# Kernel tuning notes

Measured on AMD Instinct MI355X. Metric: run time of the kernel, lower is better.

Reference implementation:

```python
import jax, jax.numpy as jnp
import numpy as np

POOL = 3      # pooling_size
EPS = 0.006   # constant added to each segment mean in the original code


def setup_inputs() -> dict:
    key = jax.random.key(0)
    k1, k2 = jax.random.split(key)
    B, N, D = 8, 3072, 1024          # N divisible by POOL -> no remainder branch
    steps = N // POOL
    x = jax.random.normal(k1, (B, N, D), dtype=jnp.float32)
    # (start, end) shot boundaries, sorted so start <= end, values in [0, N)
    graph = jnp.sort(jax.random.randint(k2, (B, steps, 2), 0, N, dtype=jnp.int64), axis=-1)
    return {"x": x, "graph": graph}


def reference(x, graph):
    B, N, D = x.shape
    steps = N // POOL
    # Exclusive+inclusive prefix sums: c[b, k] = sum over x[b, :k]  -> [B, N+1, D]
    c = jnp.concatenate([jnp.zeros((B, 1, D), x.dtype), jnp.cumsum(x, axis=1)], axis=1)
    s = graph[..., 0]                # [B, steps]
    e = graph[..., 1]                # [B, steps]
    idx_e = jnp.broadcast_to((e + 1)[..., None], (B, steps, D))
    idx_s = jnp.broadcast_to(s[..., None], (B, steps, D))
    seg_sum = jnp.take_along_axis(c, idx_e, axis=1) - jnp.take_along_axis(c, idx_s, axis=1)
    seg_len = (e - s + 1).astype(x.dtype)[..., None]
    seg_mean = seg_sum / seg_len + EPS            # [B, steps, D]
    # fixed-size window mean over consecutive POOL frames
    win_mean = x.reshape(B, steps, POOL, D).mean(axis=2)   # [B, steps, D]
    # original appends (segment mean, window mean) per step -> interleave
    out = jnp.stack([seg_mean, win_mean], axis=2).reshape(B, 2 * steps, D)
    return out
```

## Files before the change

kernel.cpp:

```cpp
#include <hip/hip_runtime.h>


constexpr int Bdim  = 8;
constexpr int Nn    = 3072;
constexpr int Dd    = 1024;
constexpr int STEPS = 1024;
constexpr int CHW   = 8;
constexpr int NCH   = 128;
constexpr int KT    = 2;
constexpr int NKT   = 512;
constexpr int D4    = Dd / 4;
constexpr float EPS = 0.006f;

constexpr size_t WL_E = (size_t)Bdim * STEPS * Dd;
constexpr size_t P_E  = (size_t)Bdim * NCH * Dd;

typedef float nat_f4 __attribute__((ext_vector_type(4)));

__device__ __forceinline__ float4 f4add(float4 a, float4 b) {
    return make_float4(a.x + b.x, a.y + b.y, a.z + b.z, a.w + b.w);
}

__device__ __forceinline__ float4 f4sel(bool c, float4 a, float4 b) {
    return make_float4(c ? a.x : b.x, c ? a.y : b.y,
                       c ? a.z : b.z, c ? a.w : b.w);
}

__device__ __forceinline__ void nt_store(float4 v, float4* p) {
    nat_f4 nv = {v.x, v.y, v.z, v.w};
    __builtin_nontemporal_store(nv, reinterpret_cast<nat_f4*>(p));
}

__device__ __forceinline__ float4 nt_load(const float4* p) {
    nat_f4 nv = __builtin_nontemporal_load(reinterpret_cast<const nat_f4*>(p));
    return make_float4(nv.x, nv.y, nv.z, nv.w);
}

__global__ __launch_bounds__(256)
void k1_scan(const float4* __restrict__ x4, float4* __restrict__ out4,
             float4* __restrict__ Wl4, float4* __restrict__ P4) {
    const int t  = threadIdx.x;
    const int ch = blockIdx.x;
    const int b  = blockIdx.y;
    const int k0 = ch * CHW;
    const int r0 = k0 * 3;

    const float4* xp = x4   + ((size_t)(b * Nn + r0)) * D4 + t;
    float4*       wl = Wl4  + ((size_t)(b * STEPS + k0)) * D4 + t;
    float4*       op = out4 + ((size_t)b * 2 * STEPS) * D4 + t;

    float4 v[3 * CHW];
#pragma unroll
    for (int i = 0; i < 3 * CHW; ++i)
        v[i] = nt_load(&xp[(size_t)i * D4]);

    float4 w[CHW];
#pragma unroll
    for (int wi = 0; wi < CHW; ++wi)
        w[wi] = f4add(f4add(v[3 * wi], v[3 * wi + 1]), v[3 * wi + 2]);

    float4 run = make_float4(0.f, 0.f, 0.f, 0.f);
#pragma unroll
    for (int wi = 0; wi < CHW; ++wi) {
        wl[(size_t)wi * D4] = run;
        float4 wm = make_float4(w[wi].x * (1.f / 3.f), w[wi].y * (1.f / 3.f),
                                w[wi].z * (1.f / 3.f), w[wi].w * (1.f / 3.f));
        nt_store(wm, &op[(size_t)(2 * (k0 + wi) + 1) * D4]);
        run = f4add(run, w[wi]);
    }
    P4[((size_t)b * NCH + ch) * D4 + t] = run;
}

__global__ __launch_bounds__(256)
void k2_chscan(const float4* __restrict__ P4, float4* __restrict__ O4) {
    __shared__ float4 part[8][33];
    const int cw  = threadIdx.x & 31;
    const int seg = threadIdx.x >> 5;
    const int col = blockIdx.x * 32 + cw;
    const int b   = blockIdx.y;

    const float4* p = P4 + (size_t)b * NCH * D4 + col;
    float4 v[16];
    float4 sum = make_float4(0.f, 0.f, 0.f, 0.f);
#pragma unroll
    for (int i = 0; i < 16; ++i) {
        v[i] = p[(size_t)(seg * 16 + i) * D4];
        sum = f4add(sum, v[i]);
    }
    part[seg][cw] = sum;
    __syncthreads();
    if (threadIdx.x < 32) {
        float4 run = make_float4(0.f, 0.f, 0.f, 0.f);
#pragma unroll
        for (int s = 0; s < 8; ++s) {
            float4 t2 = part[s][threadIdx.x];
            part[s][threadIdx.x] = run;
            run = f4add(run, t2);
        }
    }
    __syncthreads();
    float4 run = part[seg][cw];
    float4* o = O4 + (size_t)b * (NCH + 1) * D4 + col;
#pragma unroll
    for (int i = 0; i < 16; ++i) {
        o[(size_t)(seg * 16 + i) * D4] = run;
        run = f4add(run, v[i]);
    }
    if (seg == 7) o[(size_t)NCH * D4] = run;
}

__global__ __launch_bounds__(256)
void k3_gather(const float4* __restrict__ x4, const float4* __restrict__ Wl4,
               const float4* __restrict__ O4, const int* __restrict__ graph,
               float4* __restrict__ out4) {
    const int t  = threadIdx.x;
    const int kt = blockIdx.x;
    const int b  = blockIdx.y;

    const int4 g2 = *reinterpret_cast<const int4*>(
        graph + ((size_t)(b * STEPS + kt * KT)) * 2);
    const int sA[KT] = {g2.x, g2.z};
    const int eA[KT] = {g2.y, g2.w};

    const float4* xb = x4  + (size_t)b * Nn * D4 + t;
    const float4* wl = Wl4 + (size_t)b * STEPS * D4 + t;
    const float4* oc = O4  + (size_t)b * (NCH + 1) * D4 + t;
    float4*       ob = out4 + (size_t)b * 2 * STEPS * D4 + t;

    float4 o1[KT], w1[KT], xs0[KT], xs1[KT];
    float4 o2[KT], w2[KT], xe0[KT], xe1[KT];
    int r1[KT], r2[KT], ieA[KT];
    float4 tot = oc[(size_t)NCH * D4];
#pragma unroll
    for (int u = 0; u < KT; ++u) {
        int s  = sA[u];
        int m1 = s / 3;          r1[u] = s - 3 * m1;
        o1[u]  = oc[(size_t)(m1 >> 3) * D4];
        w1[u]  = wl[(size_t)m1 * D4];
        xs0[u] = xb[(size_t)(3 * m1) * D4];
        xs1[u] = xb[(size_t)(3 * m1 + 1) * D4];

        int ie = eA[u] + 1;      ieA[u] = ie;
        int m2 = ie / 3;         r2[u] = ie - 3 * m2;
        int mc = m2 < STEPS - 1 ? m2 : STEPS - 1;
        o2[u]  = oc[(size_t)(mc >> 3) * D4];
        w2[u]  = wl[(size_t)mc * D4];
        xe0[u] = xb[(size_t)(3 * mc) * D4];
        xe1[u] = xb[(size_t)(3 * mc + 1) * D4];
    }

    const float4 z4 = make_float4(0.f, 0.f, 0.f, 0.f);
#pragma unroll
    for (int u = 0; u < KT; ++u) {
        float4 cs = f4add(f4add(o1[u], w1[u]),
                          f4add(f4sel(r1[u] > 0, xs0[u], z4),
                                f4sel(r1[u] > 1, xs1[u], z4)));
        float4 ceN = f4add(f4add(o2[u], w2[u]),
                           f4add(f4sel(r2[u] > 0, xe0[u], z4),
                                 f4sel(r2[u] > 1, xe1[u], z4)));
        float4 ce = f4sel(ieA[u] == Nn, tot, ceN);

        float inv = 1.f / (float)(eA[u] - sA[u] + 1);
        float4 res = make_float4((ce.x - cs.x) * inv + EPS,
                                 (ce.y - cs.y) * inv + EPS,
                                 (ce.z - cs.z) * inv + EPS,
                                 (ce.w - cs.w) * inv + EPS);
        int k = kt * KT + u;
        nt_store(res, &ob[(size_t)(2 * k) * D4]);
    }
}

extern "C" void kernel_launch(void* const* d_in, const int* in_sizes, int n_in,
                              void* d_out, int out_size, void* d_ws, size_t ws_size,
                              hipStream_t stream) {
    const float* x     = (const float*)d_in[0];
    const int*   graph = (const int*)d_in[1];
    float*       out   = (float*)d_out;

    float* Wl = (float*)d_ws;
    float* P  = Wl + WL_E;
    float* O  = P + P_E;

    dim3 g1(NCH, Bdim);
    k1_scan<<<g1, 256, 0, stream>>>((const float4*)x, (float4*)out,
                                    (float4*)Wl, (float4*)P);
    dim3 g2(D4 / 32, Bdim);
    k2_chscan<<<g2, 256, 0, stream>>>((const float4*)P, (float4*)O);
    dim3 g3(NKT, Bdim);
    k3_gather<<<g3, 256, 0, stream>>>((const float4*)x, (const float4*)Wl,
                                      (const float4*)O, graph, (float4*)out);
}
```

Before: 192.3 us.

## Store full per-row local prefix sums so the gather needs two lookups per boundary

The first kernel now writes a chunk-local exclusive prefix sum for every input row instead of one per pooling window. Each segment boundary can then be rebuilt from a chunk offset plus a single row prefix, replacing the window-prefix plus conditional extra rows and their remainder selects. The gather kernel also handles four steps per block instead of two. The cost is a workspace three times larger and much more write traffic in the scan kernel, traded against fewer and simpler gather reads.

```diff
diff --git a/kernel.cpp b/kernel.cpp
--- a/kernel.cpp
+++ b/kernel.cpp
@@ -6,14 +6,15 @@
 constexpr int Dd    = 1024;
 constexpr int STEPS = 1024;
 constexpr int CHW   = 8;
+constexpr int CHR   = 24;
 constexpr int NCH   = 128;
-constexpr int KT    = 2;
-constexpr int NKT   = 512;
+constexpr int KT    = 4;
+constexpr int NKT   = 256;
 constexpr int D4    = Dd / 4;
 constexpr float EPS = 0.006f;
 
-constexpr size_t WL_E = (size_t)Bdim * STEPS * Dd;
-constexpr size_t P_E  = (size_t)Bdim * NCH * Dd;
+constexpr size_t R_E = (size_t)Bdim * Nn * Dd;
+constexpr size_t P_E = (size_t)Bdim * NCH * Dd;
 
 typedef float nat_f4 __attribute__((ext_vector_type(4)));
 
@@ -38,35 +39,35 @@
 
 __global__ __launch_bounds__(256)
 void k1_scan(const float4* __restrict__ x4, float4* __restrict__ out4,
-             float4* __restrict__ Wl4, float4* __restrict__ P4) {
+             float4* __restrict__ R4, float4* __restrict__ P4) {
     const int t  = threadIdx.x;
     const int ch = blockIdx.x;
     const int b  = blockIdx.y;
     const int k0 = ch * CHW;
-    const int r0 = k0 * 3;
+    const int r0 = ch * CHR;
 
     const float4* xp = x4   + ((size_t)(b * Nn + r0)) * D4 + t;
-    float4*       wl = Wl4  + ((size_t)(b * STEPS + k0)) * D4 + t;
+    float4*       rl = R4   + ((size_t)(b * Nn + r0)) * D4 + t;
     float4*       op = out4 + ((size_t)b * 2 * STEPS) * D4 + t;
 
-    float4 v[3 * CHW];
+    float4 v[CHR];
 #pragma unroll
-    for (int i = 0; i < 3 * CHW; ++i)
+    for (int i = 0; i < CHR; ++i)
         v[i] = nt_load(&xp[(size_t)i * D4]);
 
-    float4 w[CHW];
 #pragma unroll
-    for (int wi = 0; wi < CHW; ++wi)
-        w[wi] = f4add(f4add(v[3 * wi], v[3 * wi + 1]), v[3 * wi + 2]);
+    for (int wi = 0; wi < CHW; ++wi) {
+        float4 w = f4add(f4add(v[3 * wi], v[3 * wi + 1]), v[3 * wi + 2]);
+        float4 wm = make_float4(w.x * (1.f / 3.f), w.y * (1.f / 3.f),
+                                w.z * (1.f / 3.f), w.w * (1.f / 3.f));
+        nt_store(wm, &op[(size_t)(2 * (k0 + wi) + 1) * D4]);
+    }
 
     float4 run = make_float4(0.f, 0.f, 0.f, 0.f);
 #pragma unroll
-    for (int wi = 0; wi < CHW; ++wi) {
-        wl[(size_t)wi * D4] = run;
-        float4 wm = make_float4(w[wi].x * (1.f / 3.f), w[wi].y * (1.f / 3.f),
-                                w[wi].z * (1.f / 3.f), w[wi].w * (1.f / 3.f));
-        nt_store(wm, &op[(size_t)(2 * (k0 + wi) + 1) * D4]);
-        run = f4add(run, w[wi]);
+    for (int i = 0; i < CHR; ++i) {
+        rl[(size_t)i * D4] = run;
+        run = f4add(run, v[i]);
     }
     P4[((size_t)b * NCH + ch) * D4 + t] = run;
 }
@@ -110,55 +111,43 @@
 }
 
 __global__ __launch_bounds__(256)
-void k3_gather(const float4* __restrict__ x4, const float4* __restrict__ Wl4,
-               const float4* __restrict__ O4, const int* __restrict__ graph,
-               float4* __restrict__ out4) {
+void k3_gather(const float4* __restrict__ R4, const float4* __restrict__ O4,
+               const int* __restrict__ graph, float4* __restrict__ out4) {
     const int t  = threadIdx.x;
     const int kt = blockIdx.x;
     const int b  = blockIdx.y;
 
-    const int4 g2 = *reinterpret_cast<const int4*>(
-        graph + ((size_t)(b * STEPS + kt * KT)) * 2);
-    const int sA[KT] = {g2.x, g2.z};
-    const int eA[KT] = {g2.y, g2.w};
+    const int* gp = graph + ((size_t)(b * STEPS + kt * KT)) * 2;
+    const int4 ga = *reinterpret_cast<const int4*>(gp);
+    const int4 gb = *reinterpret_cast<const int4*>(gp + 4);
+    const int sA[KT] = {ga.x, ga.z, gb.x, gb.z};
+    const int eA[KT] = {ga.y, ga.w, gb.y, gb.w};
 
-    const float4* xb = x4  + (size_t)b * Nn * D4 + t;
-    const float4* wl = Wl4 + (size_t)b * STEPS * D4 + t;
+    const float4* rb = R4  + (size_t)b * Nn * D4 + t;
     const float4* oc = O4  + (size_t)b * (NCH + 1) * D4 + t;
     float4*       ob = out4 + (size_t)b * 2 * STEPS * D4 + t;
 
-    float4 o1[KT], w1[KT], xs0[KT], xs1[KT];
-    float4 o2[KT], w2[KT], xe0[KT], xe1[KT];
-    int r1[KT], r2[KT], ieA[KT];
-    float4 tot = oc[(size_t)NCH * D4];
+    float4 o1[KT], r1[KT], o2[KT], r2[KT];
+    int ieA[KT];
 #pragma unroll
     for (int u = 0; u < KT; ++u) {
         int s  = sA[u];
-        int m1 = s / 3;          r1[u] = s - 3 * m1;
-        o1[u]  = oc[(size_t)(m1 >> 3) * D4];
-        w1[u]  = wl[(size_t)m1 * D4];
-        xs0[u] = xb[(size_t)(3 * m1) * D4];
-        xs1[u] = xb[(size_t)(3 * m1 + 1) * D4];
+        int c1 = s / CHR;
+        o1[u] = oc[(size_t)c1 * D4];
+        r1[u] = rb[(size_t)s * D4];
 
         int ie = eA[u] + 1;      ieA[u] = ie;
-        int m2 = ie / 3;         r2[u] = ie - 3 * m2;
-        int mc = m2 < STEPS - 1 ? m2 : STEPS - 1;
-        o2[u]  = oc[(size_t)(mc >> 3) * D4];
-        w2[u]  = wl[(size_t)mc * D4];
-        xe0[u] = xb[(size_t)(3 * mc) * D4];
-        xe1[u] = xb[(size_t)(3 * mc + 1) * D4];
+        int c2 = ie / CHR;
+        o2[u] = oc[(size_t)c2 * D4];
+        int rc = ie < Nn ? ie : Nn - 1;
+        r2[u] = rb[(size_t)rc * D4];
     }
 
     const float4 z4 = make_float4(0.f, 0.f, 0.f, 0.f);
 #pragma unroll
     for (int u = 0; u < KT; ++u) {
-        float4 cs = f4add(f4add(o1[u], w1[u]),
-                          f4add(f4sel(r1[u] > 0, xs0[u], z4),
-                                f4sel(r1[u] > 1, xs1[u], z4)));
-        float4 ceN = f4add(f4add(o2[u], w2[u]),
-                           f4add(f4sel(r2[u] > 0, xe0[u], z4),
-                                 f4sel(r2[u] > 1, xe1[u], z4)));
-        float4 ce = f4sel(ieA[u] == Nn, tot, ceN);
+        float4 cs = f4add(o1[u], r1[u]);
+        float4 ce = f4add(o2[u], f4sel(ieA[u] < Nn, r2[u], z4));
 
         float inv = 1.f / (float)(eA[u] - sA[u] + 1);
         float4 res = make_float4((ce.x - cs.x) * inv + EPS,
@@ -177,16 +166,16 @@
     const int*   graph = (const int*)d_in[1];
     float*       out   = (float*)d_out;
 
-    float* Wl = (float*)d_ws;
-    float* P  = Wl + WL_E;
-    float* O  = P + P_E;
+    float* R = (float*)d_ws;
+    float* P = R + R_E;
+    float* O = P + P_E;
 
     dim3 g1(NCH, Bdim);
     k1_scan<<<g1, 256, 0, stream>>>((const float4*)x, (float4*)out,
-                                    (float4*)Wl, (float4*)P);
+                                    (float4*)R, (float4*)P);
     dim3 g2(D4 / 32, Bdim);
     k2_chscan<<<g2, 256, 0, stream>>>((const float4*)P, (float4*)O);
     dim3 g3(NKT, Bdim);
-    k3_gather<<<g3, 256, 0, stream>>>((const float4*)x, (const float4*)Wl,
-                                      (const float4*)O, graph, (float4*)out);
+    k3_gather<<<g3, 256, 0, stream>>>((const float4*)R, (const float4*)O,
+                                      graph, (float4*)out);
 }
```

Result: no change. 195.0 us (+1.4%).
